# Performance work log

Measured on AMD Instinct MI355X. Metric: run time of the kernel, lower is better.

The kernel has to match this reference:

```python
import jax, jax.numpy as jnp
import numpy as np

N_NODES = 50000
N_EDGES = 300000
N_ETYPES = 4
D = 256          # input_dim == output_dim (no zero-pad branch in GatedGraphConv)
RES = 768        # res_feature_dim
N_GRAPHS = 128
N_STEPS = 8
HID = 256        # classifier hidden dim


def setup_inputs() -> dict:
    key = jax.random.key(0)
    ks = jax.random.split(key, 12)
    s = 0.05
    return {
        "features": jax.random.normal(ks[0], (N_NODES, D + RES), jnp.float32),
        "W_e": jax.random.normal(ks[1], (N_ETYPES, D, D), jnp.float32) * s,
        "b_e": jnp.zeros((N_ETYPES, D), jnp.float32),
        "W_ih": jax.random.normal(ks[2], (D, 3 * D), jnp.float32) * s,
        "W_hh": jax.random.normal(ks[3], (D, 3 * D), jnp.float32) * s,
        "b_ih": jnp.zeros((3 * D,), jnp.float32),
        "b_hh": jnp.zeros((3 * D,), jnp.float32),
        "W1": jax.random.normal(ks[4], (D + RES, HID), jnp.float32) * s,
        "b1": jnp.zeros((HID,), jnp.float32),
        "W2": jax.random.normal(ks[5], (HID, 1), jnp.float32) * s,
        "b2": jnp.zeros((1,), jnp.float32),
        "src": jax.random.randint(ks[6], (N_EDGES,), 0, N_NODES),
        "dst": jax.random.randint(ks[7], (N_EDGES,), 0, N_NODES),
        "etypes": jax.random.randint(ks[8], (N_EDGES,), 0, N_ETYPES),
        "node2graph": jnp.sort(jax.random.randint(ks[9], (N_NODES,), 0, N_GRAPHS)),
    }


def _gru_cell(x, h, W_ih, W_hh, b_ih, b_hh):
    # PyTorch GRUCell, gate order (r, z, n)
    gi = x @ W_ih + b_ih
    gh = h @ W_hh + b_hh
    i_r, i_z, i_n = jnp.split(gi, 3, axis=-1)
    h_r, h_z, h_n = jnp.split(gh, 3, axis=-1)
    r = jax.nn.sigmoid(i_r + h_r)
    z = jax.nn.sigmoid(i_z + h_z)
    n = jnp.tanh(i_n + r * h_n)
    return (1.0 - z) * n + z * h


def reference(features, W_e, b_e, W_ih, W_hh, b_ih, b_hh, W1, b1, W2, b2,
              src, dst, etypes, node2graph):
    h = features[:, :D]          # node features fed to GGNN
    res = features[:, D:]        # mixed residual features (bypass GGNN)

    def step(h, _):
        # per-edge-type linear on all nodes: [T, N, D]
        ht = jnp.einsum('nd,tde->tne', h, W_e) + b_e[:, None, :]
        msgs = ht[etypes, src]                                   # [E, D]
        a = jax.ops.segment_sum(msgs, dst, num_segments=N_NODES)  # scatter-add to dst
        return _gru_cell(a, h, W_ih, W_hh, b_ih, b_hh), None

    h, _ = jax.lax.scan(step, h, None, length=N_STEPS)

    out = jnp.concatenate([h, res], axis=1)  # [N, D+RES]
    # masked mean over nodes of each graph == segment mean
    sums = jax.ops.segment_sum(out, node2graph, num_segments=N_GRAPHS)
    cnts = jax.ops.segment_sum(jnp.ones((N_NODES,), out.dtype), node2graph,
                               num_segments=N_GRAPHS)
    pooled = sums / jnp.maximum(cnts, 1.0)[:, None]  # [B, D+RES]

    # classifier (dropouts inactive at eval): Linear -> ReLU -> Linear -> sigmoid
    hcls = jax.nn.relu(pooled @ W1 + b1)
    logits = hcls @ W2 + b2
    return jax.nn.sigmoid(logits)  # [B, 1]
```

## Files before the change

### kernel.cpp

```cpp
#include <hip/hip_runtime.h>
#include <math.h>
#include <stdint.h>

#define NN 50000
#define NE 300000
#define NT4 200000
#define NG 128
#define NSTEP 8
#define MPAD 50048
#define SCB 196
#define SCB2 782
#define PCH 8
#define EM 64
#define ECAP 896

#define BM 128
#define BN 128
#define BK 64

typedef __attribute__((ext_vector_type(8))) short bf16x8;
typedef __attribute__((ext_vector_type(8))) unsigned short u16x8;
typedef __attribute__((ext_vector_type(4))) float f32x4;
typedef unsigned short u16;
typedef unsigned int u32;

__device__ __forceinline__ float b2f(u16 u) {
  union { u32 i; float f; } c; c.i = ((u32)u) << 16; return c.f;
}
__device__ __forceinline__ u16 f2b(float f) {
  union { float f; u32 i; } c; c.f = f;
  u32 x = c.i;
  u32 r = (x + 0x7fffu + ((x >> 16) & 1u)) >> 16;
  return (u16)r;
}

__device__ __forceinline__ void load_lds16(const void* g, void* l) {
  __builtin_amdgcn_global_load_lds((const __attribute__((address_space(1))) u32*)g,
                                   (__attribute__((address_space(3))) u32*)l, 16, 0, 0);
}

__global__ void k_conv_we(const float* __restrict__ W_e, u16* __restrict__ Wt) {
  int i = blockIdx.x * 256 + threadIdx.x;
  int c = i >> 8, d = i & 255;
  Wt[c * 256 + d] = f2b(W_e[(c >> 8) * 65536 + d * 256 + (c & 255)]);
}
__global__ void k_conv_rz(const float* __restrict__ W_ih, const float* __restrict__ W_hh,
                          u16* __restrict__ ah, u16* __restrict__ ha) {
  int i = blockIdx.x * 256 + threadIdx.x;
  int n = i >> 9, k = i & 511;
  float va = (k < 256) ? W_ih[k * 768 + n] : W_hh[(k - 256) * 768 + n];
  float vh = (k < 256) ? W_hh[k * 768 + n] : W_ih[(k - 256) * 768 + n];
  ah[n * 512 + k] = f2b(va);
  ha[n * 512 + k] = f2b(vh);
}
__global__ void k_conv_n(const float* __restrict__ W, u16* __restrict__ Wt) {
  int i = blockIdx.x * 256 + threadIdx.x;
  int n = i >> 8, k = i & 255;
  Wt[n * 256 + k] = f2b(W[k * 768 + 512 + n]);
}
__global__ void k_brz(const float* __restrict__ b_ih, const float* __restrict__ b_hh,
                      float* __restrict__ b_rz) {
  int i = blockIdx.x * 256 + threadIdx.x;
  if (i < 512) b_rz[i] = b_ih[i] + b_hh[i];
}

__global__ void k_init_h(const float* __restrict__ feat, u16* __restrict__ acat) {
  int i = blockIdx.x * 256 + threadIdx.x;
  int n = i >> 6, d = (i & 63) << 2;
  ushort4 o;
  if (n < NN) {
    float4 v = *(const float4*)(feat + (size_t)n * 1024 + d);
    o.x = f2b(v.x); o.y = f2b(v.y); o.z = f2b(v.z); o.w = f2b(v.w);
  } else {
    o.x = o.y = o.z = o.w = 0;
  }
  *(ushort4*)(acat + (size_t)n * 768 + d) = o;
}

__global__ void k_hist(const int* __restrict__ dst, const int* __restrict__ ety,
                       int* __restrict__ deg2) {
  int e = blockIdx.x * 256 + threadIdx.x;
  if (e < NE) atomicAdd(&deg2[dst[e] * 4 + ety[e]], 1);
}
__global__ void k_scan1(const int* __restrict__ deg2, int* __restrict__ part, int* __restrict__ bsum) {
  __shared__ int sh[256];
  int b = blockIdx.x, t = threadIdx.x;
  int i = b * 256 + t;
  int v = (i < NT4) ? deg2[i] : 0;
  sh[t] = v;
  __syncthreads();
  for (int off = 1; off < 256; off <<= 1) {
    int tmp = (t >= off) ? sh[t - off] : 0;
    __syncthreads();
    sh[t] += tmp;
    __syncthreads();
  }
  if (i < NT4) part[i] = sh[t] - v;
  if (t == 255) bsum[b] = sh[255];
}
__global__ void k_scan2(const int* __restrict__ bsum, int* __restrict__ boff) {
  __shared__ int sh[1024];
  int t = threadIdx.x;
  int v = (t < SCB2) ? bsum[t] : 0;
  sh[t] = v;
  __syncthreads();
  for (int off = 1; off < 1024; off <<= 1) {
    int tmp = (t >= off) ? sh[t - off] : 0;
    __syncthreads();
    sh[t] += tmp;
    __syncthreads();
  }
  boff[t] = sh[t] - v;
  if (t == 1023) boff[1024] = sh[1023];
}
__global__ void k_scan3(const int* __restrict__ part, const int* __restrict__ boff, int* __restrict__ rp2) {
  int i = blockIdx.x * 256 + threadIdx.x;
  if (i < NT4) rp2[i] = part[i] + boff[i >> 8];
  if (i == NT4) rp2[NT4] = boff[1024];
}
__global__ void k_scatter(const int* __restrict__ src, const int* __restrict__ dst,
                          const int* __restrict__ ety, const int* __restrict__ rp2,
                          int* __restrict__ cursor2, int* __restrict__ esrc) {
  int e = blockIdx.x * 256 + threadIdx.x;
  if (e < NE) {
    int seg = dst[e] * 4 + ety[e];
    int p = rp2[seg] + atomicAdd(&cursor2[seg], 1);
    esrc[p] = src[e];
  }
}
__global__ void k_cnt2(const int* __restrict__ deg2, ushort4* __restrict__ cnt2) {
  int v = blockIdx.x * 256 + threadIdx.x;
  if (v >= MPAD) return;
  ushort4 o;
  if (v < NN) {
    o.x = (u16)deg2[v * 4 + 0]; o.y = (u16)deg2[v * 4 + 1];
    o.z = (u16)deg2[v * 4 + 2]; o.w = (u16)deg2[v * 4 + 3];
  } else {
    o.x = o.y = o.z = o.w = 0;
  }
  cnt2[v] = o;
}
__global__ void k_gstart(const int* __restrict__ n2g, int* __restrict__ gstart) {
  int n = blockIdx.x * 256 + threadIdx.x;
  if (n >= NN) return;
  int g = n2g[n];
  int gp = (n == 0) ? -1 : n2g[n - 1];
  for (int x = gp + 1; x <= g; ++x) gstart[x] = n;
  if (n == NN - 1)
    for (int x = g + 1; x <= NG; ++x) gstart[x] = NN;
}

__global__ __launch_bounds__(512, 4) void k_eagg(
    const u16* __restrict__ acat, int hboff,
    const int* __restrict__ rp2, const int* __restrict__ esrc,
    const u16* __restrict__ Wt_e, const u16* __restrict__ Wt_in,
    const ushort4* __restrict__ cnt2, const float* __restrict__ b_e,
    const float* __restrict__ b_ih512,
    u16* __restrict__ acat_out, u16* __restrict__ inb) {
  __shared__ __align__(16) char Ss[EM * 512];
  __shared__ __align__(16) char Bs[256 * 128];
  __shared__ int Es[ECAP];
  __shared__ int Rp[257];
  const int tid = threadIdx.x;
  const int wv = tid >> 6, l = tid & 63;
  const int hw = tid >> 5, lw = tid & 31;
  const int m0 = blockIdx.x * EM;
  const int fr = l & 15, kq = l >> 4;
  const int wm = (wv >> 2) * 32, wn = (wv & 3) * 64;

  const int base4 = m0 * 4;
  const int e0 = rp2[base4];
  for (int i = tid; i <= 256; i += 512) {
    int idx = base4 + i;
    if (idx > NT4) idx = NT4;
    Rp[i] = rp2[idx] - e0;
  }
  {
    int idxe = base4 + 256;
    if (idxe > NT4) idxe = NT4;
    int ecnt = rp2[idxe] - e0;
    int ecl = ecnt < ECAP ? ecnt : ECAP;
    for (int i = tid; i < ecl; i += 512) Es[i] = esrc[e0 + i] * 768 + hboff;
  }
  __syncthreads();

  f32x4 acc[2][4];
#pragma unroll
  for (int m = 0; m < 2; ++m)
#pragma unroll
    for (int n = 0; n < 4; ++n) acc[m][n] = (f32x4){0.f, 0.f, 0.f, 0.f};

  for (int t = 0; t < 4; ++t) {
    if (t > 0) __syncthreads();
    int cc[4], ee[4];
#pragma unroll
    for (int rr = 0; rr < 4; ++rr) {
      int li = (hw * 4 + rr) * 4 + t;
      cc[rr] = Rp[li];
      ee[rr] = Rp[li + 1];
    }
    float ar[4][8];
#pragma unroll
    for (int rr = 0; rr < 4; ++rr)
#pragma unroll
      for (int q = 0; q < 8; ++q) ar[rr][q] = 0.f;
    bool more = (cc[0] < ee[0]) | (cc[1] < ee[1]) | (cc[2] < ee[2]) | (cc[3] < ee[3]);
    while (more) {
      u16x8 v[4];
      bool p[4];
#pragma unroll
      for (int rr = 0; rr < 4; ++rr) {
        p[rr] = cc[rr] < ee[rr];
        if (p[rr]) {
          int rel = cc[rr];
          int off = (rel < ECAP) ? Es[rel] : (esrc[e0 + rel] * 768 + hboff);
          v[rr] = *(const u16x8*)(acat + (size_t)off + lw * 8);
        }
      }
#pragma unroll
      for (int rr = 0; rr < 4; ++rr) {
        if (p[rr]) {
#pragma unroll
          for (int q = 0; q < 8; ++q) ar[rr][q] += b2f(v[rr][q]);
          cc[rr]++;
        }
      }
      more = (cc[0] < ee[0]) | (cc[1] < ee[1]) | (cc[2] < ee[2]) | (cc[3] < ee[3]);
    }
#pragma unroll
    for (int rr = 0; rr < 4; ++rr) {
      int row = hw * 4 + rr;
      u16x8 o;
#pragma unroll
      for (int q = 0; q < 8; ++q) o[q] = f2b(ar[rr][q]);
      *(u16x8*)(Ss + row * 512 + ((lw * 16) ^ ((row & 7) << 4))) = o;
    }

    const u16* Bw = Wt_e + (size_t)t * 65536;
    for (int kc = 0; kc < 4; ++kc) {
      __syncthreads();
#pragma unroll
      for (int pph = 0; pph < 4; ++pph) {
        int brow = pph * 64 + (tid >> 3);
        int ks = kc * 64 + (((tid & 7) ^ (brow & 7)) << 3);
        load_lds16(Bw + (size_t)brow * 256 + ks, Bs + pph * 8192 + wv * 1024);
      }
      asm volatile("s_waitcnt vmcnt(0)" ::: "memory");
      __syncthreads();
#pragma unroll
      for (int kk = 0; kk < 64; kk += 32) {
        bf16x8 af[2], bfr[4];
        int kb = (kk + kq * 8) * 2;
        int ka = (kc * 64 + kk + kq * 8) * 2;
#pragma unroll
        for (int m = 0; m < 2; ++m) {
          int R = wm + m * 16 + fr;
          af[m] = *(const bf16x8*)(Ss + R * 512 + (ka ^ ((R & 7) << 4)));
        }
#pragma unroll
        for (int n = 0; n < 4; ++n) {
          int R = wn + n * 16 + fr;
          bfr[n] = *(const bf16x8*)(Bs + R * 128 + (kb ^ ((R & 7) << 4)));
        }
#pragma unroll
        for (int m = 0; m < 2; ++m)
#pragma unroll
          for (int n = 0; n < 4; ++n)
            acc[m][n] = __builtin_amdgcn_mfma_f32_16x16x32_bf16(af[m], bfr[n], acc[m][n], 0, 0, 0);
      }
    }
  }
  __syncthreads();

  float bev[4][4];
#pragma unroll
  for (int n = 0; n < 4; ++n)
#pragma unroll
    for (int t = 0; t < 4; ++t) bev[n][t] = b_e[t * 256 + wn + n * 16 + fr];
#pragma unroll
  for (int m = 0; m < 2; ++m) {
#pragma unroll
    for (int j = 0; j < 4; ++j) {
      int r = wm + m * 16 + kq * 4 + j;
      int v = m0 + r;
      ushort4 c4 = cnt2[v];
      float c0 = c4.x, c1 = c4.y, c2 = c4.z, c3 = c4.w;
#pragma unroll
      for (int n = 0; n < 4; ++n) {
        int col = wn + n * 16 + fr;
        float val = acc[m][n][j] + c0 * bev[n][0] + c1 * bev[n][1] + c2 * bev[n][2] + c3 * bev[n][3];
        u16 vb = f2b(val);
        acat_out[(size_t)v * 768 + 256 + col] = vb;
        *(u16*)(Ss + r * 512 + ((col * 2) ^ ((r & 7) << 4))) = vb;
      }
    }
  }
#pragma unroll
  for (int m = 0; m < 2; ++m)
#pragma unroll
    for (int n = 0; n < 4; ++n) acc[m][n] = (f32x4){0.f, 0.f, 0.f, 0.f};

  for (int kc = 0; kc < 4; ++kc) {
    __syncthreads();
#pragma unroll
    for (int pph = 0; pph < 4; ++pph) {
      int brow = pph * 64 + (tid >> 3);
      int ks = kc * 64 + (((tid & 7) ^ (brow & 7)) << 3);
      load_lds16(Wt_in + (size_t)brow * 256 + ks, Bs + pph * 8192 + wv * 1024);
    }
    asm volatile("s_waitcnt vmcnt(0)" ::: "memory");
    __syncthreads();
#pragma unroll
    for (int kk = 0; kk < 64; kk += 32) {
      bf16x8 af[2], bfr[4];
      int kb = (kk + kq * 8) * 2;
      int ka = (kc * 64 + kk + kq * 8) * 2;
#pragma unroll
      for (int m = 0; m < 2; ++m) {
        int R = wm + m * 16 + fr;
        af[m] = *(const bf16x8*)(Ss + R * 512 + (ka ^ ((R & 7) << 4)));
      }
#pragma unroll
      for (int n = 0; n < 4; ++n) {
        int R = wn + n * 16 + fr;
        bfr[n] = *(const bf16x8*)(Bs + R * 128 + (kb ^ ((R & 7) << 4)));
      }
#pragma unroll
      for (int m = 0; m < 2; ++m)
#pragma unroll
        for (int n = 0; n < 4; ++n)
          acc[m][n] = __builtin_amdgcn_mfma_f32_16x16x32_bf16(af[m], bfr[n], acc[m][n], 0, 0, 0);
    }
  }
  float bi[4];
#pragma unroll
  for (int n = 0; n < 4; ++n) bi[n] = b_ih512[wn + n * 16 + fr];
#pragma unroll
  for (int m = 0; m < 2; ++m) {
#pragma unroll
    for (int j = 0; j < 4; ++j) {
      int v = m0 + wm + m * 16 + kq * 4 + j;
#pragma unroll
      for (int n = 0; n < 4; ++n) {
        int col = wn + n * 16 + fr;
        inb[(size_t)v * 256 + col] = f2b(acc[m][n][j] + bi[n]);
      }
    }
  }
}

template <int MODE>
__global__ __launch_bounds__(256, 2) void k_gemm(const u16* __restrict__ A, int lda, int K,
                                                 const u16* __restrict__ Bt,
                                                 const float* __restrict__ bias,
                                                 u16* __restrict__ C, int ldc,
                                                 const u16* __restrict__ rzb,
                                                 const u16* __restrict__ inb,
                                                 const u16* __restrict__ hold,
                                                 u16* __restrict__ hnew) {
  __shared__ __align__(16) char lds[(BM + BN) * BK * 2];
  char* As = lds;
  char* Bs = lds + BM * BK * 2;
  const int tid = threadIdx.x;
  const int w = tid >> 6, l = tid & 63;
  const int m0 = blockIdx.y * BM, n0 = blockIdx.x * BN;
  const int rld = tid >> 3;
  const int cld = tid & 7;
  const int wm = (w >> 1) * 64, wn = (w & 1) * 64;
  const int fr = l & 15, kq = l >> 4;
  f32x4 acc[4][4];
#pragma unroll
  for (int m = 0; m < 4; ++m)
#pragma unroll
    for (int n = 0; n < 4; ++n) acc[m][n] = (f32x4){0.f, 0.f, 0.f, 0.f};

  for (int k0 = 0; k0 < K; k0 += BK) {
#pragma unroll
    for (int p = 0; p < 4; ++p) {
      int row = p * 32 + rld;
      int ks = k0 + ((cld ^ (row & 7)) << 3);
      load_lds16(A + (size_t)(m0 + row) * lda + ks, As + p * 4096 + w * 1024);
    }
#pragma unroll
    for (int p = 0; p < 4; ++p) {
      int row = p * 32 + rld;
      int ks = k0 + ((cld ^ (row & 7)) << 3);
      load_lds16(Bt + (size_t)(n0 + row) * K + ks, Bs + p * 4096 + w * 1024);
    }
    asm volatile("s_waitcnt vmcnt(0)" ::: "memory");
    __syncthreads();
#pragma unroll
    for (int kk = 0; kk < BK; kk += 32) {
      bf16x8 af[4], bfr[4];
      int kb = (kk + kq * 8) * 2;
#pragma unroll
      for (int m = 0; m < 4; ++m) {
        int R = wm + m * 16 + fr;
        af[m] = *(const bf16x8*)(As + R * 128 + (kb ^ ((R & 7) << 4)));
      }
#pragma unroll
      for (int n = 0; n < 4; ++n) {
        int R = wn + n * 16 + fr;
        bfr[n] = *(const bf16x8*)(Bs + R * 128 + (kb ^ ((R & 7) << 4)));
      }
#pragma unroll
      for (int m = 0; m < 4; ++m)
#pragma unroll
        for (int n = 0; n < 4; ++n)
          acc[m][n] = __builtin_amdgcn_mfma_f32_16x16x32_bf16(af[m], bfr[n], acc[m][n], 0, 0, 0);
    }
    __syncthreads();
  }
#pragma unroll
  for (int m = 0; m < 4; ++m) {
#pragma unroll
    for (int n = 0; n < 4; ++n) {
      int col = n0 + wn + n * 16 + fr;
      float bv = bias[col];
#pragma unroll
      for (int j = 0; j < 4; ++j) {
        int row = m0 + wm + m * 16 + kq * 4 + j;
        float v = acc[m][n][j] + bv;
        if (MODE == 1) {
          C[(size_t)row * ldc + col] = f2b(1.f / (1.f + expf(-v)));
        } else {
          float r = b2f(rzb[(size_t)row * 512 + col]);
          float z = b2f(rzb[(size_t)row * 512 + 256 + col]);
          float in_ = b2f(inb[(size_t)row * 256 + col]);
          float ho = b2f(hold[(size_t)row * 768 + col]);
          float ng = tanhf(in_ + r * v);
          float hv = (1.f - z) * ng + z * ho;
          hnew[(size_t)row * 768 + col] = f2b(hv);
        }
      }
    }
  }
}

__global__ __launch_bounds__(256) void k_pool(const u16* __restrict__ hb, const float* __restrict__ feat,
                                              const int* __restrict__ gstart, float* __restrict__ pooled) {
  int g = blockIdx.x, ch = blockIdx.y, t = threadIdx.x;
  int s = gstart[g], e = gstart[g + 1];
  int tot = e - s;
  int per = (tot + PCH - 1) / PCH;
  int ns = s + ch * per;
  int ne = ns + per < e ? ns + per : e;
  if (ns >= ne) return;
  int c = t << 2;
  float a0 = 0.f, a1 = 0.f, a2 = 0.f, a3 = 0.f;
  if (c < 256) {
    for (int n = ns; n < ne; ++n) {
      ushort4 u = *(const ushort4*)(hb + (size_t)n * 768 + c);
      a0 += b2f(u.x); a1 += b2f(u.y); a2 += b2f(u.z); a3 += b2f(u.w);
    }
  } else {
    for (int n = ns; n < ne; ++n) {
      float4 v = *(const float4*)(feat + (size_t)n * 1024 + c);
      a0 += v.x; a1 += v.y; a2 += v.z; a3 += v.w;
    }
  }
  atomicAdd(&pooled[g * 1024 + c], a0);
  atomicAdd(&pooled[g * 1024 + c + 1], a1);
  atomicAdd(&pooled[g * 1024 + c + 2], a2);
  atomicAdd(&pooled[g * 1024 + c + 3], a3);
}

__global__ __launch_bounds__(256) void k_head(const float* __restrict__ pooled,
                                              const int* __restrict__ gstart,
                                              const float* __restrict__ W1, const float* __restrict__ b1,
                                              const float* __restrict__ W2, const float* __restrict__ b2,
                                              float* __restrict__ out) {
  __shared__ float sp[1024];
  __shared__ float red[256];
  int g = blockIdx.x, t = threadIdx.x;
  float inv = 1.f / fmaxf((float)(gstart[g + 1] - gstart[g]), 1.f);
  for (int i = t; i < 1024; i += 256) sp[i] = pooled[g * 1024 + i] * inv;
  __syncthreads();
  float acc = b1[t];
  for (int k = 0; k < 1024; ++k) acc += sp[k] * W1[k * 256 + t];
  float hc = fmaxf(acc, 0.f);
  red[t] = hc * W2[t];
  __syncthreads();
  for (int s2 = 128; s2 > 0; s2 >>= 1) {
    if (t < s2) red[t] += red[t + s2];
    __syncthreads();
  }
  if (t == 0) out[g] = 1.f / (1.f + expf(-(red[0] + b2[0])));
}

extern "C" void kernel_launch(void* const* d_in, const int* in_sizes, int n_in, void* d_out, int out_size,
                              void* d_ws, size_t ws_size, hipStream_t stream) {
  const float* feat = (const float*)d_in[0];
  const float* W_e = (const float*)d_in[1];
  const float* b_e = (const float*)d_in[2];
  const float* W_ih = (const float*)d_in[3];
  const float* W_hh = (const float*)d_in[4];
  const float* b_ih = (const float*)d_in[5];
  const float* b_hh = (const float*)d_in[6];
  const float* W1 = (const float*)d_in[7];
  const float* b1 = (const float*)d_in[8];
  const float* W2 = (const float*)d_in[9];
  const float* b2 = (const float*)d_in[10];
  const int* src = (const int*)d_in[11];
  const int* dst = (const int*)d_in[12];
  const int* ety = (const int*)d_in[13];
  const int* n2g = (const int*)d_in[14];

  char* p = (char*)d_ws;
  auto alloc = [&](size_t b) { char* r = p; p += (b + 255) & ~(size_t)255; return r; };
  u16* acat = (u16*)alloc((size_t)MPAD * 768 * 2);
  u16* rzb = (u16*)alloc((size_t)MPAD * 512 * 2);
  u16* inb = (u16*)alloc((size_t)MPAD * 256 * 2);
  u16* Wt_e = (u16*)alloc(1024 * 256 * 2);
  u16* Wt_rz_ah = (u16*)alloc(512 * 512 * 2);
  u16* Wt_rz_ha = (u16*)alloc(512 * 512 * 2);
  u16* Wt_in = (u16*)alloc(256 * 256 * 2);
  u16* Wt_hn = (u16*)alloc(256 * 256 * 2);
  float* b_rz = (float*)alloc(512 * 4);
  int* deg2 = (int*)alloc((size_t)NT4 * 4);
  int* part = (int*)alloc((size_t)NT4 * 4);
  int* bsum = (int*)alloc((size_t)SCB2 * 4);
  int* boff = (int*)alloc(1025 * 4);
  int* rp2 = (int*)alloc((size_t)(NT4 + 1) * 4);
  int* cursor2 = (int*)alloc((size_t)NT4 * 4);
  int* esrc = (int*)alloc((size_t)NE * 4);
  ushort4* cnt2 = (ushort4*)alloc((size_t)MPAD * 8);
  int* gstart = (int*)alloc((size_t)(NG + 1) * 4);
  float* pooled = (float*)alloc((size_t)NG * 1024 * 4);

  hipMemsetAsync(deg2, 0, (size_t)NT4 * 4, stream);
  hipMemsetAsync(cursor2, 0, (size_t)NT4 * 4, stream);
  hipMemsetAsync(pooled, 0, (size_t)NG * 1024 * 4, stream);

  k_conv_we<<<1024, 256, 0, stream>>>(W_e, Wt_e);
  k_conv_rz<<<1024, 256, 0, stream>>>(W_ih, W_hh, Wt_rz_ah, Wt_rz_ha);
  k_conv_n<<<256, 256, 0, stream>>>(W_ih, Wt_in);
  k_conv_n<<<256, 256, 0, stream>>>(W_hh, Wt_hn);
  k_brz<<<2, 256, 0, stream>>>(b_ih, b_hh, b_rz);
  k_init_h<<<MPAD / 4, 256, 0, stream>>>(feat, acat);
  k_hist<<<(NE + 255) / 256, 256, 0, stream>>>(dst, ety, deg2);
  k_scan1<<<SCB2, 256, 0, stream>>>(deg2, part, bsum);
  k_scan2<<<1, 1024, 0, stream>>>(bsum, boff);
  k_scan3<<<SCB2 + 1, 256, 0, stream>>>(part, boff, rp2);
  k_scatter<<<(NE + 255) / 256, 256, 0, stream>>>(src, dst, ety, rp2, cursor2, esrc);
  k_cnt2<<<(MPAD + 255) / 256, 256, 0, stream>>>(deg2, cnt2);
  k_gstart<<<SCB, 256, 0, stream>>>(n2g, gstart);

  for (int s = 0; s < NSTEP; ++s) {
    int hboff = (s & 1) ? 512 : 0;
    int hnewoff = 512 - hboff;
    int rzoff = (s & 1) ? 256 : 0;
    const u16* Wrz = (s & 1) ? Wt_rz_ah : Wt_rz_ha;
    k_eagg<<<MPAD / EM, 512, 0, stream>>>(acat, hboff, rp2, esrc, Wt_e, Wt_in, cnt2, b_e,
                                          b_ih + 512, acat, inb);
    k_gemm<1><<<dim3(512 / BN, MPAD / BM), 256, 0, stream>>>(
        acat + rzoff, 768, 512, Wrz, b_rz, rzb, 512, nullptr, nullptr, nullptr, nullptr);
    k_gemm<2><<<dim3(256 / BN, MPAD / BM), 256, 0, stream>>>(
        acat + hboff, 768, 256, Wt_hn, b_hh + 512, nullptr, 0, rzb, inb, acat + hboff,
        acat + hnewoff);
  }

  k_pool<<<dim3(NG, PCH), 256, 0, stream>>>(acat, feat, gstart, pooled);
  k_head<<<NG, 256, 0, stream>>>(pooled, gstart, W1, b1, W2, b2, (float*)d_out);
}
```

Before: 1.729 ms.

## Fuse GRU gate GEMMs into one kernel and read edge weights from global

The two per-step GEMM kernels (r/z gates and new-gate) and the input-gate GEMM previously done inside the edge aggregation kernel are merged into a single k_gru2 kernel. Each 64-row block stages both halves of the concatenated activations in LDS once and computes r, z, i_n and h_n accumulators together. The GRU update is applied in the epilogue, so the rzb and inb intermediate buffers disappear. The edge-aggregation kernel now reads W_e fragments straight from global/L2 instead of staging them through LDS, which drops its B buffer and the barriers around it. In exchange, k_gru2 uses a large LDS footprint and many accumulator registers, and the direct global weight reads may be less efficient.

```diff
diff --git a/kernel.cpp b/kernel.cpp
--- a/kernel.cpp
+++ b/kernel.cpp
@@ -14,10 +14,6 @@
 #define EM 64
 #define ECAP 896
 
-#define BM 128
-#define BN 128
-#define BK 64
-
 typedef __attribute__((ext_vector_type(8))) short bf16x8;
 typedef __attribute__((ext_vector_type(8))) unsigned short u16x8;
 typedef __attribute__((ext_vector_type(4))) float f32x4;
@@ -153,12 +149,10 @@
 __global__ __launch_bounds__(512, 4) void k_eagg(
     const u16* __restrict__ acat, int hboff,
     const int* __restrict__ rp2, const int* __restrict__ esrc,
-    const u16* __restrict__ Wt_e, const u16* __restrict__ Wt_in,
+    const u16* __restrict__ Wt_e,
     const ushort4* __restrict__ cnt2, const float* __restrict__ b_e,
-    const float* __restrict__ b_ih512,
-    u16* __restrict__ acat_out, u16* __restrict__ inb) {
+    u16* __restrict__ acat_out) {
   __shared__ __align__(16) char Ss[EM * 512];
-  __shared__ __align__(16) char Bs[256 * 128];
   __shared__ int Es[ECAP];
   __shared__ int Rp[257];
   const int tid = threadIdx.x;
@@ -235,42 +229,30 @@
       for (int q = 0; q < 8; ++q) o[q] = f2b(ar[rr][q]);
       *(u16x8*)(Ss + row * 512 + ((lw * 16) ^ ((row & 7) << 4))) = o;
     }
+    __syncthreads();
 
     const u16* Bw = Wt_e + (size_t)t * 65536;
-    for (int kc = 0; kc < 4; ++kc) {
-      __syncthreads();
-#pragma unroll
-      for (int pph = 0; pph < 4; ++pph) {
-        int brow = pph * 64 + (tid >> 3);
-        int ks = kc * 64 + (((tid & 7) ^ (brow & 7)) << 3);
-        load_lds16(Bw + (size_t)brow * 256 + ks, Bs + pph * 8192 + wv * 1024);
-      }
-      asm volatile("s_waitcnt vmcnt(0)" ::: "memory");
-      __syncthreads();
-#pragma unroll
-      for (int kk = 0; kk < 64; kk += 32) {
-        bf16x8 af[2], bfr[4];
-        int kb = (kk + kq * 8) * 2;
-        int ka = (kc * 64 + kk + kq * 8) * 2;
-#pragma unroll
-        for (int m = 0; m < 2; ++m) {
-          int R = wm + m * 16 + fr;
-          af[m] = *(const bf16x8*)(Ss + R * 512 + (ka ^ ((R & 7) << 4)));
-        }
-#pragma unroll
-        for (int n = 0; n < 4; ++n) {
-          int R = wn + n * 16 + fr;
-          bfr[n] = *(const bf16x8*)(Bs + R * 128 + (kb ^ ((R & 7) << 4)));
-        }
-#pragma unroll
-        for (int m = 0; m < 2; ++m)
-#pragma unroll
-          for (int n = 0; n < 4; ++n)
-            acc[m][n] = __builtin_amdgcn_mfma_f32_16x16x32_bf16(af[m], bfr[n], acc[m][n], 0, 0, 0);
-      }
-    }
-  }
-  __syncthreads();
+#pragma unroll 2
+    for (int k8 = 0; k8 < 8; ++k8) {
+      bf16x8 af[2], bfr[4];
+      int ka = (k8 * 32 + kq * 8) * 2;
+#pragma unroll
+      for (int m = 0; m < 2; ++m) {
+        int R = wm + m * 16 + fr;
+        af[m] = *(const bf16x8*)(Ss + R * 512 + (ka ^ ((R & 7) << 4)));
+      }
+#pragma unroll
+      for (int n = 0; n < 4; ++n) {
+        int R = wn + n * 16 + fr;
+        bfr[n] = *(const bf16x8*)(Bw + (size_t)R * 256 + k8 * 32 + kq * 8);
+      }
+#pragma unroll
+      for (int m = 0; m < 2; ++m)
+#pragma unroll
+        for (int n = 0; n < 4; ++n)
+          acc[m][n] = __builtin_amdgcn_mfma_f32_16x16x32_bf16(af[m], bfr[n], acc[m][n], 0, 0, 0);
+    }
+  }
 
   float bev[4][4];
 #pragma unroll
@@ -281,157 +263,160 @@
   for (int m = 0; m < 2; ++m) {
 #pragma unroll
     for (int j = 0; j < 4; ++j) {
-      int r = wm + m * 16 + kq * 4 + j;
-      int v = m0 + r;
+      int rl = wm + m * 16 + kq * 4 + j;
+      int v = m0 + rl;
       ushort4 c4 = cnt2[v];
       float c0 = c4.x, c1 = c4.y, c2 = c4.z, c3 = c4.w;
 #pragma unroll
       for (int n = 0; n < 4; ++n) {
         int col = wn + n * 16 + fr;
         float val = acc[m][n][j] + c0 * bev[n][0] + c1 * bev[n][1] + c2 * bev[n][2] + c3 * bev[n][3];
-        u16 vb = f2b(val);
-        acat_out[(size_t)v * 768 + 256 + col] = vb;
-        *(u16*)(Ss + r * 512 + ((col * 2) ^ ((r & 7) << 4))) = vb;
-      }
-    }
-  }
+        acat_out[(size_t)v * 768 + 256 + col] = f2b(val);
+      }
+    }
+  }
+}
+
+__global__ __launch_bounds__(512, 2) void k_gru2(
+    const u16* __restrict__ acat, int rzoff, int hnewoff, int swap,
+    const u16* __restrict__ Wrz, const u16* __restrict__ Wt_in, const u16* __restrict__ Wt_hn,
+    const float* __restrict__ b_rz, const float* __restrict__ b_ih, const float* __restrict__ b_hh,
+    u16* __restrict__ acat_out) {
+  __shared__ __align__(16) char As1[64 * 512];
+  __shared__ __align__(16) char As2[64 * 512];
+  __shared__ __align__(16) char Bs[512 * 128];
+  const int tid = threadIdx.x;
+  const int wv = tid >> 6, l = tid & 63;
+  const int m0 = blockIdx.x * 64;
+  const int fr = l & 15, kq = l >> 4;
+  const int wm = (wv >> 2) * 32, wn = (wv & 3) * 64;
+
+#pragma unroll
+  for (int p = 0; p < 4; ++p) {
+    int row = p * 16 + wv * 2 + (l >> 5);
+    int ksrc = ((l & 31) ^ (row & 7)) << 3;
+    load_lds16(acat + (size_t)(m0 + row) * 768 + rzoff + ksrc, As1 + p * 8192 + wv * 1024);
+    load_lds16(acat + (size_t)(m0 + row) * 768 + rzoff + 256 + ksrc, As2 + p * 8192 + wv * 1024);
+  }
+
+  f32x4 ar_[2][4], az_[2][4], ai_[2][4], ah_[2][4];
 #pragma unroll
   for (int m = 0; m < 2; ++m)
 #pragma unroll
-    for (int n = 0; n < 4; ++n) acc[m][n] = (f32x4){0.f, 0.f, 0.f, 0.f};
-
-  for (int kc = 0; kc < 4; ++kc) {
-    __syncthreads();
-#pragma unroll
-    for (int pph = 0; pph < 4; ++pph) {
-      int brow = pph * 64 + (tid >> 3);
-      int ks = kc * 64 + (((tid & 7) ^ (brow & 7)) << 3);
-      load_lds16(Wt_in + (size_t)brow * 256 + ks, Bs + pph * 8192 + wv * 1024);
+    for (int n = 0; n < 4; ++n) {
+      ar_[m][n] = (f32x4){0.f, 0.f, 0.f, 0.f};
+      az_[m][n] = (f32x4){0.f, 0.f, 0.f, 0.f};
+      ai_[m][n] = (f32x4){0.f, 0.f, 0.f, 0.f};
+      ah_[m][n] = (f32x4){0.f, 0.f, 0.f, 0.f};
+    }
+
+  for (int kc = 0; kc < 8; ++kc) {
+#pragma unroll
+    for (int p = 0; p < 8; ++p) {
+      int brow = p * 64 + wv * 8 + (l >> 3);
+      int ks = kc * 64 + (((l & 7) ^ (brow & 7)) << 3);
+      load_lds16(Wrz + (size_t)brow * 512 + ks, Bs + p * 8192 + wv * 1024);
     }
     asm volatile("s_waitcnt vmcnt(0)" ::: "memory");
     __syncthreads();
+    const char* Asrc = (kc < 4) ? As1 : As2;
+    int kbase = (kc & 3) * 64;
 #pragma unroll
     for (int kk = 0; kk < 64; kk += 32) {
-      bf16x8 af[2], bfr[4];
+      bf16x8 af[2], br4[4], bz4[4];
+      int ka = (kbase + kk + kq * 8) * 2;
       int kb = (kk + kq * 8) * 2;
-      int ka = (kc * 64 + kk + kq * 8) * 2;
 #pragma unroll
       for (int m = 0; m < 2; ++m) {
         int R = wm + m * 16 + fr;
-        af[m] = *(const bf16x8*)(Ss + R * 512 + (ka ^ ((R & 7) << 4)));
+        af[m] = *(const bf16x8*)(Asrc + R * 512 + (ka ^ ((R & 7) << 4)));
       }
 #pragma unroll
       for (int n = 0; n < 4; ++n) {
-        int R = wn + n * 16 + fr;
-        bfr[n] = *(const bf16x8*)(Bs + R * 128 + (kb ^ ((R & 7) << 4)));
+        int Rr = wn + n * 16 + fr;
+        int Rz = Rr + 256;
+        br4[n] = *(const bf16x8*)(Bs + Rr * 128 + (kb ^ ((Rr & 7) << 4)));
+        bz4[n] = *(const bf16x8*)(Bs + Rz * 128 + (kb ^ ((Rz & 7) << 4)));
       }
 #pragma unroll
       for (int m = 0; m < 2; ++m)
 #pragma unroll
-        for (int n = 0; n < 4; ++n)
-          acc[m][n] = __builtin_amdgcn_mfma_f32_16x16x32_bf16(af[m], bfr[n], acc[m][n], 0, 0, 0);
-    }
-  }
-  float bi[4];
-#pragma unroll
-  for (int n = 0; n < 4; ++n) bi[n] = b_ih512[wn + n * 16 + fr];
+        for (int n = 0; n < 4; ++n) {
+          ar_[m][n] = __builtin_amdgcn_mfma_f32_16x16x32_bf16(af[m], br4[n], ar_[m][n], 0, 0, 0);
+          az_[m][n] = __builtin_amdgcn_mfma_f32_16x16x32_bf16(af[m], bz4[n], az_[m][n], 0, 0, 0);
+        }
+    }
+    __syncthreads();
+  }
+
+  const char* Asa = swap ? As1 : As2;
+  const char* Ash = swap ? As2 : As1;
+  for (int kc = 0; kc < 4; ++kc) {
+#pragma unroll
+    for (int p = 0; p < 8; ++p) {
+      int brow = p * 64 + wv * 8 + (l >> 3);
+      const u16* srcw = (brow < 256) ? (Wt_in + (size_t)brow * 256)
+                                     : (Wt_hn + (size_t)(brow - 256) * 256);
+      int ks = kc * 64 + (((l & 7) ^ (brow & 7)) << 3);
+      load_lds16(srcw + ks, Bs + p * 8192 + wv * 1024);
+    }
+    asm volatile("s_waitcnt vmcnt(0)" ::: "memory");
+    __syncthreads();
+    int kbase = kc * 64;
+#pragma unroll
+    for (int kk = 0; kk < 64; kk += 32) {
+      bf16x8 afa[2], afh[2], bi4[4], bh4[4];
+      int ka = (kbase + kk + kq * 8) * 2;
+      int kb = (kk + kq * 8) * 2;
+#pragma unroll
+      for (int m = 0; m < 2; ++m) {
+        int R = wm + m * 16 + fr;
+        afa[m] = *(const bf16x8*)(Asa + R * 512 + (ka ^ ((R & 7) << 4)));
+        afh[m] = *(const bf16x8*)(Ash + R * 512 + (ka ^ ((R & 7) << 4)));
+      }
+#pragma unroll
+      for (int n = 0; n < 4; ++n) {
+        int Ri = wn + n * 16 + fr;
+        int Rh = Ri + 256;
+        bi4[n] = *(const bf16x8*)(Bs + Ri * 128 + (kb ^ ((Ri & 7) << 4)));
+        bh4[n] = *(const bf16x8*)(Bs + Rh * 128 + (kb ^ ((Rh & 7) << 4)));
+      }
+#pragma unroll
+      for (int m = 0; m < 2; ++m)
+#pragma unroll
+        for (int n = 0; n < 4; ++n) {
+          ai_[m][n] = __builtin_amdgcn_mfma_f32_16x16x32_bf16(afa[m], bi4[n], ai_[m][n], 0, 0, 0);
+          ah_[m][n] = __builtin_amdgcn_mfma_f32_16x16x32_bf16(afh[m], bh4[n], ah_[m][n], 0, 0, 0);
+        }
+    }
+    __syncthreads();
+  }
+
+  float brb[4], bzb[4], bib[4], bhb[4];
+#pragma unroll
+  for (int n = 0; n < 4; ++n) {
+    int c = wn + n * 16 + fr;
+    brb[n] = b_rz[c];
+    bzb[n] = b_rz[256 + c];
+    bib[n] = b_ih[512 + c];
+    bhb[n] = b_hh[512 + c];
+  }
 #pragma unroll
   for (int m = 0; m < 2; ++m) {
 #pragma unroll
     for (int j = 0; j < 4; ++j) {
-      int v = m0 + wm + m * 16 + kq * 4 + j;
+      int rl = wm + m * 16 + kq * 4 + j;
+      int v = m0 + rl;
 #pragma unroll
       for (int n = 0; n < 4; ++n) {
-        int col = wn + n * 16 + fr;
-        inb[(size_t)v * 256 + col] = f2b(acc[m][n][j] + bi[n]);
-      }
-    }
-  }
-}
-
-template <int MODE>
-__global__ __launch_bounds__(256, 2) void k_gemm(const u16* __restrict__ A, int lda, int K,
-                                                 const u16* __restrict__ Bt,
-                                                 const float* __restrict__ bias,
-                                                 u16* __restrict__ C, int ldc,
-                                                 const u16* __restrict__ rzb,
-                                                 const u16* __restrict__ inb,
-                                                 const u16* __restrict__ hold,
-                                                 u16* __restrict__ hnew) {
-  __shared__ __align__(16) char lds[(BM + BN) * BK * 2];
-  char* As = lds;
-  char* Bs = lds + BM * BK * 2;
-  const int tid = threadIdx.x;
-  const int w = tid >> 6, l = tid & 63;
-  const int m0 = blockIdx.y * BM, n0 = blockIdx.x * BN;
-  const int rld = tid >> 3;
-  const int cld = tid & 7;
-  const int wm = (w >> 1) * 64, wn = (w & 1) * 64;
-  const int fr = l & 15, kq = l >> 4;
-  f32x4 acc[4][4];
-#pragma unroll
-  for (int m = 0; m < 4; ++m)
-#pragma unroll
-    for (int n = 0; n < 4; ++n) acc[m][n] = (f32x4){0.f, 0.f, 0.f, 0.f};
-
-  for (int k0 = 0; k0 < K; k0 += BK) {
-#pragma unroll
-    for (int p = 0; p < 4; ++p) {
-      int row = p * 32 + rld;
-      int ks = k0 + ((cld ^ (row & 7)) << 3);
-      load_lds16(A + (size_t)(m0 + row) * lda + ks, As + p * 4096 + w * 1024);
-    }
-#pragma unroll
-    for (int p = 0; p < 4; ++p) {
-      int row = p * 32 + rld;
-      int ks = k0 + ((cld ^ (row & 7)) << 3);
-      load_lds16(Bt + (size_t)(n0 + row) * K + ks, Bs + p * 4096 + w * 1024);
-    }
-    asm volatile("s_waitcnt vmcnt(0)" ::: "memory");
-    __syncthreads();
-#pragma unroll
-    for (int kk = 0; kk < BK; kk += 32) {
-      bf16x8 af[4], bfr[4];
-      int kb = (kk + kq * 8) * 2;
-#pragma unroll
-      for (int m = 0; m < 4; ++m) {
-        int R = wm + m * 16 + fr;
-        af[m] = *(const bf16x8*)(As + R * 128 + (kb ^ ((R & 7) << 4)));
-      }
-#pragma unroll
-      for (int n = 0; n < 4; ++n) {
-        int R = wn + n * 16 + fr;
-        bfr[n] = *(const bf16x8*)(Bs + R * 128 + (kb ^ ((R & 7) << 4)));
-      }
-#pragma unroll
-      for (int m = 0; m < 4; ++m)
-#pragma unroll
-        for (int n = 0; n < 4; ++n)
-          acc[m][n] = __builtin_amdgcn_mfma_f32_16x16x32_bf16(af[m], bfr[n], acc[m][n], 0, 0, 0);
-    }
-    __syncthreads();
-  }
-#pragma unroll
-  for (int m = 0; m < 4; ++m) {
-#pragma unroll
-    for (int n = 0; n < 4; ++n) {
-      int col = n0 + wn + n * 16 + fr;
-      float bv = bias[col];
-#pragma unroll
-      for (int j = 0; j < 4; ++j) {
-        int row = m0 + wm + m * 16 + kq * 4 + j;
-        float v = acc[m][n][j] + bv;
-        if (MODE == 1) {
-          C[(size_t)row * ldc + col] = f2b(1.f / (1.f + expf(-v)));
-        } else {
-          float r = b2f(rzb[(size_t)row * 512 + col]);
-          float z = b2f(rzb[(size_t)row * 512 + 256 + col]);
-          float in_ = b2f(inb[(size_t)row * 256 + col]);
-          float ho = b2f(hold[(size_t)row * 768 + col]);
-          float ng = tanhf(in_ + r * v);
-          float hv = (1.f - z) * ng + z * ho;
-          hnew[(size_t)row * 768 + col] = f2b(hv);
-        }
+        int c = wn + n * 16 + fr;
+        float r = 1.f / (1.f + expf(-(ar_[m][n][j] + brb[n])));
+        float z = 1.f / (1.f + expf(-(az_[m][n][j] + bzb[n])));
+        float in_ = ai_[m][n][j] + bib[n];
+        float hn_ = ah_[m][n][j] + bhb[n];
+        float ho = b2f(*(const u16*)(Ash + rl * 512 + ((c * 2) ^ ((rl & 7) << 4))));
+        float ng = tanhf(in_ + r * hn_);
+        acat_out[(size_t)v * 768 + hnewoff + c] = f2b((1.f - z) * ng + z * ho);
       }
     }
   }
@@ -509,8 +494,6 @@
   char* p = (char*)d_ws;
   auto alloc = [&](size_t b) { char* r = p; p += (b + 255) & ~(size_t)255; return r; };
   u16* acat = (u16*)alloc((size_t)MPAD * 768 * 2);
-  u16* rzb = (u16*)alloc((size_t)MPAD * 512 * 2);
-  u16* inb = (u16*)alloc((size_t)MPAD * 256 * 2);
   u16* Wt_e = (u16*)alloc(1024 * 256 * 2);
   u16* Wt_rz_ah = (u16*)alloc(512 * 512 * 2);
   u16* Wt_rz_ha = (u16*)alloc(512 * 512 * 2);
@@ -550,14 +533,11 @@
     int hboff = (s & 1) ? 512 : 0;
     int hnewoff = 512 - hboff;
     int rzoff = (s & 1) ? 256 : 0;
+    int swap = s & 1;
     const u16* Wrz = (s & 1) ? Wt_rz_ah : Wt_rz_ha;
-    k_eagg<<<MPAD / EM, 512, 0, stream>>>(acat, hboff, rp2, esrc, Wt_e, Wt_in, cnt2, b_e,
-                                          b_ih + 512, acat, inb);
-    k_gemm<1><<<dim3(512 / BN, MPAD / BM), 256, 0, stream>>>(
-        acat + rzoff, 768, 512, Wrz, b_rz, rzb, 512, nullptr, nullptr, nullptr, nullptr);
-    k_gemm<2><<<dim3(256 / BN, MPAD / BM), 256, 0, stream>>>(
-        acat + hboff, 768, 256, Wt_hn, b_hh + 512, nullptr, 0, rzb, inb, acat + hboff,
-        acat + hnewoff);
+    k_eagg<<<MPAD / EM, 512, 0, stream>>>(acat, hboff, rp2, esrc, Wt_e, cnt2, b_e, acat);
+    k_gru2<<<MPAD / 64, 512, 0, stream>>>(acat, rzoff, hnewoff, swap, Wrz, Wt_in, Wt_hn,
+                                          b_rz, b_ih, b_hh, acat);
   }
 
   k_pool<<<dim3(NG, PCH), 256, 0, stream>>>(acat, feat, gstart, pooled);
```

After: 2.305 ms. +33.3%, slower.

## Shrink edge-aggregation blocks, read weights directly, split input-gate GEMM into separate kernel

Applied to the files above, without the earlier changes.

The edge aggregation kernel now handles 32 nodes per block with 256 threads instead of 64 with 512. It drops the LDS staging of the per-type weights and loads the B fragments straight from global memory, with no K-chunk barriers. The fused input-gate (n) projection is moved out into a new plain GEMM mode launched as its own kernel. This aims to reduce LDS use and synchronization and raise occupancy, at the cost of an extra launch and rereading the aggregated messages from global memory.

```diff
diff --git a/kernel.cpp b/kernel.cpp
--- a/kernel.cpp
+++ b/kernel.cpp
@@ -11,8 +11,8 @@
 #define SCB 196
 #define SCB2 782
 #define PCH 8
-#define EM 64
-#define ECAP 896
+#define EM 32
+#define ECAP2 512
 
 #define BM 128
 #define BN 128
@@ -150,45 +150,42 @@
     for (int x = g + 1; x <= NG; ++x) gstart[x] = NN;
 }
 
-__global__ __launch_bounds__(512, 4) void k_eagg(
+__global__ __launch_bounds__(256, 4) void k_eagg(
     const u16* __restrict__ acat, int hboff,
     const int* __restrict__ rp2, const int* __restrict__ esrc,
-    const u16* __restrict__ Wt_e, const u16* __restrict__ Wt_in,
+    const u16* __restrict__ Wt_e,
     const ushort4* __restrict__ cnt2, const float* __restrict__ b_e,
-    const float* __restrict__ b_ih512,
-    u16* __restrict__ acat_out, u16* __restrict__ inb) {
+    u16* __restrict__ acat_out) {
   __shared__ __align__(16) char Ss[EM * 512];
-  __shared__ __align__(16) char Bs[256 * 128];
-  __shared__ int Es[ECAP];
-  __shared__ int Rp[257];
+  __shared__ int Es[ECAP2];
+  __shared__ int Rp[EM * 4 + 1];
   const int tid = threadIdx.x;
   const int wv = tid >> 6, l = tid & 63;
   const int hw = tid >> 5, lw = tid & 31;
   const int m0 = blockIdx.x * EM;
   const int fr = l & 15, kq = l >> 4;
-  const int wm = (wv >> 2) * 32, wn = (wv & 3) * 64;
+  const int wm = (wv >> 1) * 16, wn = (wv & 1) * 128;
 
   const int base4 = m0 * 4;
   const int e0 = rp2[base4];
-  for (int i = tid; i <= 256; i += 512) {
+  for (int i = tid; i <= EM * 4; i += 256) {
     int idx = base4 + i;
     if (idx > NT4) idx = NT4;
     Rp[i] = rp2[idx] - e0;
   }
+  int ecnt;
   {
-    int idxe = base4 + 256;
+    int idxe = base4 + EM * 4;
     if (idxe > NT4) idxe = NT4;
-    int ecnt = rp2[idxe] - e0;
-    int ecl = ecnt < ECAP ? ecnt : ECAP;
-    for (int i = tid; i < ecl; i += 512) Es[i] = esrc[e0 + i] * 768 + hboff;
+    ecnt = rp2[idxe] - e0;
+    int ecl = ecnt < ECAP2 ? ecnt : ECAP2;
+    for (int i = tid; i < ecl; i += 256) Es[i] = esrc[e0 + i] * 768 + hboff;
   }
   __syncthreads();
 
-  f32x4 acc[2][4];
-#pragma unroll
-  for (int m = 0; m < 2; ++m)
-#pragma unroll
-    for (int n = 0; n < 4; ++n) acc[m][n] = (f32x4){0.f, 0.f, 0.f, 0.f};
+  f32x4 acc[8];
+#pragma unroll
+  for (int n = 0; n < 8; ++n) acc[n] = (f32x4){0.f, 0.f, 0.f, 0.f};
 
   for (int t = 0; t < 4; ++t) {
     if (t > 0) __syncthreads();
@@ -213,7 +210,7 @@
         p[rr] = cc[rr] < ee[rr];
         if (p[rr]) {
           int rel = cc[rr];
-          int off = (rel < ECAP) ? Es[rel] : (esrc[e0 + rel] * 768 + hboff);
+          int off = (rel < ECAP2) ? Es[rel] : (esrc[e0 + rel] * 768 + hboff);
           v[rr] = *(const u16x8*)(acat + (size_t)off + lw * 8);
         }
       }
@@ -235,116 +232,40 @@
       for (int q = 0; q < 8; ++q) o[q] = f2b(ar[rr][q]);
       *(u16x8*)(Ss + row * 512 + ((lw * 16) ^ ((row & 7) << 4))) = o;
     }
+    __syncthreads();
 
     const u16* Bw = Wt_e + (size_t)t * 65536;
-    for (int kc = 0; kc < 4; ++kc) {
-      __syncthreads();
-#pragma unroll
-      for (int pph = 0; pph < 4; ++pph) {
-        int brow = pph * 64 + (tid >> 3);
-        int ks = kc * 64 + (((tid & 7) ^ (brow & 7)) << 3);
-        load_lds16(Bw + (size_t)brow * 256 + ks, Bs + pph * 8192 + wv * 1024);
-      }
-      asm volatile("s_waitcnt vmcnt(0)" ::: "memory");
-      __syncthreads();
-#pragma unroll
-      for (int kk = 0; kk < 64; kk += 32) {
-        bf16x8 af[2], bfr[4];
-        int kb = (kk + kq * 8) * 2;
-        int ka = (kc * 64 + kk + kq * 8) * 2;
-#pragma unroll
-        for (int m = 0; m < 2; ++m) {
-          int R = wm + m * 16 + fr;
-          af[m] = *(const bf16x8*)(Ss + R * 512 + (ka ^ ((R & 7) << 4)));
-        }
-#pragma unroll
-        for (int n = 0; n < 4; ++n) {
-          int R = wn + n * 16 + fr;
-          bfr[n] = *(const bf16x8*)(Bs + R * 128 + (kb ^ ((R & 7) << 4)));
-        }
-#pragma unroll
-        for (int m = 0; m < 2; ++m)
-#pragma unroll
-          for (int n = 0; n < 4; ++n)
-            acc[m][n] = __builtin_amdgcn_mfma_f32_16x16x32_bf16(af[m], bfr[n], acc[m][n], 0, 0, 0);
-      }
-    }
-  }
-  __syncthreads();
-
-  float bev[4][4];
-#pragma unroll
-  for (int n = 0; n < 4; ++n)
-#pragma unroll
-    for (int t = 0; t < 4; ++t) bev[n][t] = b_e[t * 256 + wn + n * 16 + fr];
-#pragma unroll
-  for (int m = 0; m < 2; ++m) {
-#pragma unroll
-    for (int j = 0; j < 4; ++j) {
-      int r = wm + m * 16 + kq * 4 + j;
-      int v = m0 + r;
-      ushort4 c4 = cnt2[v];
-      float c0 = c4.x, c1 = c4.y, c2 = c4.z, c3 = c4.w;
-#pragma unroll
-      for (int n = 0; n < 4; ++n) {
-        int col = wn + n * 16 + fr;
-        float val = acc[m][n][j] + c0 * bev[n][0] + c1 * bev[n][1] + c2 * bev[n][2] + c3 * bev[n][3];
-        u16 vb = f2b(val);
-        acat_out[(size_t)v * 768 + 256 + col] = vb;
-        *(u16*)(Ss + r * 512 + ((col * 2) ^ ((r & 7) << 4))) = vb;
-      }
-    }
-  }
-#pragma unroll
-  for (int m = 0; m < 2; ++m)
-#pragma unroll
-    for (int n = 0; n < 4; ++n) acc[m][n] = (f32x4){0.f, 0.f, 0.f, 0.f};
-
-  for (int kc = 0; kc < 4; ++kc) {
-    __syncthreads();
-#pragma unroll
-    for (int pph = 0; pph < 4; ++pph) {
-      int brow = pph * 64 + (tid >> 3);
-      int ks = kc * 64 + (((tid & 7) ^ (brow & 7)) << 3);
-      load_lds16(Wt_in + (size_t)brow * 256 + ks, Bs + pph * 8192 + wv * 1024);
-    }
-    asm volatile("s_waitcnt vmcnt(0)" ::: "memory");
-    __syncthreads();
-#pragma unroll
-    for (int kk = 0; kk < 64; kk += 32) {
-      bf16x8 af[2], bfr[4];
-      int kb = (kk + kq * 8) * 2;
-      int ka = (kc * 64 + kk + kq * 8) * 2;
-#pragma unroll
-      for (int m = 0; m < 2; ++m) {
-        int R = wm + m * 16 + fr;
-        af[m] = *(const bf16x8*)(Ss + R * 512 + (ka ^ ((R & 7) << 4)));
-      }
-#pragma unroll
-      for (int n = 0; n < 4; ++n) {
+#pragma unroll
+    for (int k8 = 0; k8 < 8; ++k8) {
+      bf16x8 bfr[8], af;
+#pragma unroll
+      for (int n = 0; n < 8; ++n) {
         int R = wn + n * 16 + fr;
-        bfr[n] = *(const bf16x8*)(Bs + R * 128 + (kb ^ ((R & 7) << 4)));
-      }
-#pragma unroll
-      for (int m = 0; m < 2; ++m)
-#pragma unroll
-        for (int n = 0; n < 4; ++n)
-          acc[m][n] = __builtin_amdgcn_mfma_f32_16x16x32_bf16(af[m], bfr[n], acc[m][n], 0, 0, 0);
-    }
-  }
-  float bi[4];
-#pragma unroll
-  for (int n = 0; n < 4; ++n) bi[n] = b_ih512[wn + n * 16 + fr];
-#pragma unroll
-  for (int m = 0; m < 2; ++m) {
-#pragma unroll
-    for (int j = 0; j < 4; ++j) {
-      int v = m0 + wm + m * 16 + kq * 4 + j;
-#pragma unroll
-      for (int n = 0; n < 4; ++n) {
-        int col = wn + n * 16 + fr;
-        inb[(size_t)v * 256 + col] = f2b(acc[m][n][j] + bi[n]);
-      }
+        bfr[n] = *(const bf16x8*)(Bw + (size_t)R * 256 + k8 * 32 + kq * 8);
+      }
+      {
+        int R = wm + fr;
+        int ka = (k8 * 32 + kq * 8) * 2;
+        af = *(const bf16x8*)(Ss + R * 512 + (ka ^ ((R & 7) << 4)));
+      }
+#pragma unroll
+      for (int n = 0; n < 8; ++n)
+        acc[n] = __builtin_amdgcn_mfma_f32_16x16x32_bf16(af, bfr[n], acc[n], 0, 0, 0);
+    }
+  }
+
+#pragma unroll
+  for (int j = 0; j < 4; ++j) {
+    int rl = wm + kq * 4 + j;
+    int v = m0 + rl;
+    ushort4 c4 = cnt2[v];
+    float c0 = c4.x, c1 = c4.y, c2 = c4.z, c3 = c4.w;
+#pragma unroll
+    for (int n = 0; n < 8; ++n) {
+      int col = wn + n * 16 + fr;
+      float val = acc[n][j] + c0 * b_e[col] + c1 * b_e[256 + col] + c2 * b_e[512 + col] +
+                  c3 * b_e[768 + col];
+      acat_out[(size_t)v * 768 + 256 + col] = f2b(val);
     }
   }
 }
@@ -421,7 +342,9 @@
       for (int j = 0; j < 4; ++j) {
         int row = m0 + wm + m * 16 + kq * 4 + j;
         float v = acc[m][n][j] + bv;
-        if (MODE == 1) {
+        if (MODE == 0) {
+          C[(size_t)row * ldc + col] = f2b(v);
+        } else if (MODE == 1) {
           C[(size_t)row * ldc + col] = f2b(1.f / (1.f + expf(-v)));
         } else {
           float r = b2f(rzb[(size_t)row * 512 + col]);
@@ -551,10 +474,11 @@
     int hnewoff = 512 - hboff;
     int rzoff = (s & 1) ? 256 : 0;
     const u16* Wrz = (s & 1) ? Wt_rz_ah : Wt_rz_ha;
-    k_eagg<<<MPAD / EM, 512, 0, stream>>>(acat, hboff, rp2, esrc, Wt_e, Wt_in, cnt2, b_e,
-                                          b_ih + 512, acat, inb);
+    k_eagg<<<MPAD / EM, 256, 0, stream>>>(acat, hboff, rp2, esrc, Wt_e, cnt2, b_e, acat);
     k_gemm<1><<<dim3(512 / BN, MPAD / BM), 256, 0, stream>>>(
         acat + rzoff, 768, 512, Wrz, b_rz, rzb, 512, nullptr, nullptr, nullptr, nullptr);
+    k_gemm<0><<<dim3(256 / BN, MPAD / BM), 256, 0, stream>>>(
+        acat + 256, 768, 256, Wt_in, b_ih + 512, inb, 256, nullptr, nullptr, nullptr, nullptr);
     k_gemm<2><<<dim3(256 / BN, MPAD / BM), 256, 0, stream>>>(
         acat + hboff, 768, 256, Wt_hn, b_hh + 512, nullptr, 0, rzb, inb, acat + hboff,
         acat + hnewoff);
```

After: 3.203 ms. 85.2% more time.

## Double-buffer LDS in GRU GEMMs and narrow N tile to 64

Applied to the files above, without the earlier changes.

Restructures k_gemm to stage the next K-slice into a second LDS buffer while MFMAs run on the current one, using partial vmcnt waits and raw barriers instead of a full drain each iteration. The N tile shrinks from 128 to 64, which halves the accumulators and doubles the grid, and launch bounds rise to 3 blocks per CU for more occupancy. The cost is more LDS per block and re-reading the A tile once per extra N block.

```diff
diff --git a/kernel.cpp b/kernel.cpp
--- a/kernel.cpp
+++ b/kernel.cpp
@@ -13,10 +13,6 @@
 #define PCH 8
 #define EM 64
 #define ECAP 896
-
-#define BM 128
-#define BN 128
-#define BK 64
 
 typedef __attribute__((ext_vector_type(8))) short bf16x8;
 typedef __attribute__((ext_vector_type(8))) unsigned short u16x8;
@@ -350,7 +346,7 @@
 }
 
 template <int MODE>
-__global__ __launch_bounds__(256, 2) void k_gemm(const u16* __restrict__ A, int lda, int K,
+__global__ __launch_bounds__(256, 3) void k_gemm(const u16* __restrict__ A, int lda, int K,
                                                  const u16* __restrict__ Bt,
                                                  const float* __restrict__ bias,
                                                  u16* __restrict__ C, int ldc,
@@ -358,40 +354,53 @@
                                                  const u16* __restrict__ inb,
                                                  const u16* __restrict__ hold,
                                                  u16* __restrict__ hnew) {
-  __shared__ __align__(16) char lds[(BM + BN) * BK * 2];
-  char* As = lds;
-  char* Bs = lds + BM * BK * 2;
+  __shared__ __align__(16) char AsB[2][128 * 128];
+  __shared__ __align__(16) char BsB[2][64 * 128];
   const int tid = threadIdx.x;
   const int w = tid >> 6, l = tid & 63;
-  const int m0 = blockIdx.y * BM, n0 = blockIdx.x * BN;
+  const int m0 = blockIdx.y * 128, n0 = blockIdx.x * 64;
   const int rld = tid >> 3;
   const int cld = tid & 7;
-  const int wm = (w >> 1) * 64, wn = (w & 1) * 64;
+  const int wm = (w >> 1) * 64, wn = (w & 1) * 32;
   const int fr = l & 15, kq = l >> 4;
-  f32x4 acc[4][4];
+  f32x4 acc[4][2];
 #pragma unroll
   for (int m = 0; m < 4; ++m)
 #pragma unroll
-    for (int n = 0; n < 4; ++n) acc[m][n] = (f32x4){0.f, 0.f, 0.f, 0.f};
-
-  for (int k0 = 0; k0 < K; k0 += BK) {
+    for (int n = 0; n < 2; ++n) acc[m][n] = (f32x4){0.f, 0.f, 0.f, 0.f};
+
+  auto stage = [&](int buf, int k0) {
 #pragma unroll
     for (int p = 0; p < 4; ++p) {
       int row = p * 32 + rld;
-      int ks = k0 + ((cld ^ (row & 7)) << 3);
-      load_lds16(A + (size_t)(m0 + row) * lda + ks, As + p * 4096 + w * 1024);
-    }
-#pragma unroll
-    for (int p = 0; p < 4; ++p) {
+      load_lds16(A + (size_t)(m0 + row) * lda + k0 + ((cld ^ (row & 7)) << 3),
+                 AsB[buf] + p * 4096 + w * 1024);
+    }
+#pragma unroll
+    for (int p = 0; p < 2; ++p) {
       int row = p * 32 + rld;
-      int ks = k0 + ((cld ^ (row & 7)) << 3);
-      load_lds16(Bt + (size_t)(n0 + row) * K + ks, Bs + p * 4096 + w * 1024);
-    }
-    asm volatile("s_waitcnt vmcnt(0)" ::: "memory");
-    __syncthreads();
-#pragma unroll
-    for (int kk = 0; kk < BK; kk += 32) {
-      bf16x8 af[4], bfr[4];
+      load_lds16(Bt + (size_t)(n0 + row) * K + k0 + ((cld ^ (row & 7)) << 3),
+                 BsB[buf] + p * 4096 + w * 1024);
+    }
+  };
+
+  stage(0, 0);
+  const int NK = K >> 6;
+  for (int ki = 0; ki < NK; ++ki) {
+    const int cur = ki & 1;
+    if (ki + 1 < NK) {
+      stage(cur ^ 1, (ki + 1) << 6);
+      asm volatile("s_waitcnt vmcnt(6)" ::: "memory");
+    } else {
+      asm volatile("s_waitcnt vmcnt(0)" ::: "memory");
+    }
+    __builtin_amdgcn_s_barrier();
+    __builtin_amdgcn_sched_barrier(0);
+    const char* As = AsB[cur];
+    const char* Bs = BsB[cur];
+#pragma unroll
+    for (int kk = 0; kk < 64; kk += 32) {
+      bf16x8 af[4], bfr[2];
       int kb = (kk + kq * 8) * 2;
 #pragma unroll
       for (int m = 0; m < 4; ++m) {
@@ -399,22 +408,25 @@
         af[m] = *(const bf16x8*)(As + R * 128 + (kb ^ ((R & 7) << 4)));
       }
 #pragma unroll
-      for (int n = 0; n < 4; ++n) {
+      for (int n = 0; n < 2; ++n) {
         int R = wn + n * 16 + fr;
         bfr[n] = *(const bf16x8*)(Bs + R * 128 + (kb ^ ((R & 7) << 4)));
       }
 #pragma unroll
       for (int m = 0; m < 4; ++m)
 #pragma unroll
-        for (int n = 0; n < 4; ++n)
+        for (int n = 0; n < 2; ++n)
           acc[m][n] = __builtin_amdgcn_mfma_f32_16x16x32_bf16(af[m], bfr[n], acc[m][n], 0, 0, 0);
     }
-    __syncthreads();
-  }
+    asm volatile("s_waitcnt lgkmcnt(0)" ::: "memory");
+    __builtin_amdgcn_sched_barrier(0);
+    __builtin_amdgcn_s_barrier();
+  }
+
 #pragma unroll
   for (int m = 0; m < 4; ++m) {
 #pragma unroll
-    for (int n = 0; n < 4; ++n) {
+    for (int n = 0; n < 2; ++n) {
       int col = n0 + wn + n * 16 + fr;
       float bv = bias[col];
 #pragma unroll
@@ -553,9 +565,9 @@
     const u16* Wrz = (s & 1) ? Wt_rz_ah : Wt_rz_ha;
     k_eagg<<<MPAD / EM, 512, 0, stream>>>(acat, hboff, rp2, esrc, Wt_e, Wt_in, cnt2, b_e,
                                           b_ih + 512, acat, inb);
-    k_gemm<1><<<dim3(512 / BN, MPAD / BM), 256, 0, stream>>>(
+    k_gemm<1><<<dim3(512 / 64, MPAD / 128), 256, 0, stream>>>(
         acat + rzoff, 768, 512, Wrz, b_rz, rzb, 512, nullptr, nullptr, nullptr, nullptr);
-    k_gemm<2><<<dim3(256 / BN, MPAD / BM), 256, 0, stream>>>(
+    k_gemm<2><<<dim3(256 / 64, MPAD / 128), 256, 0, stream>>>(
         acat + hboff, 768, 256, Wt_hn, b_hh + 512, nullptr, 0, rzb, inb, acat + hboff,
         acat + hnewoff);
   }
```

New measurement: 1.887 ms. 9.1% more time.
